# Performance work log

Measured on AMD Instinct MI355X. Metric: run time of the kernel, lower is better.

The kernel has to match this reference:

```python
import jax, jax.numpy as jnp
import numpy as np

N, E, IN, H, ED = 50000, 800000, 128, 128, 3
EPS = 1e-5

def _gat_conv(x, src, dst, ea, W, a_src, a_dst, We, a_edge, bias):
    n = x.shape[0]
    # add self loops; self-loop edge_attr = per-feature mean (PyG fill_value='mean')
    loops = jnp.arange(n, dtype=src.dtype)
    s = jnp.concatenate([src, loops])
    d = jnp.concatenate([dst, loops])
    ea_full = jnp.concatenate([ea, jnp.broadcast_to(ea.mean(0), (n, ea.shape[1]))], 0)
    h = x @ W                       # [n, H]
    al_s = h @ a_src                # [n]
    al_d = h @ a_dst
    al_e = (ea_full @ We) @ a_edge  # [E+n]
    alpha = jax.nn.leaky_relu(al_s[s] + al_d[d] + al_e, 0.2)
    # segment softmax over destination nodes (every node has a self loop)
    amax = jax.ops.segment_max(alpha, d, num_segments=n)
    ex = jnp.exp(alpha - amax[d])
    denom = jax.ops.segment_sum(ex, d, num_segments=n)
    coef = ex / (denom[d] + 1e-16)
    out = jax.ops.segment_sum(h[s] * coef[:, None], d, num_segments=n)
    return out + bias

def _bn(x, gamma, beta):
    mu = x.mean(0)
    var = ((x - mu) ** 2).mean(0)
    return (x - mu) * jax.lax.rsqrt(var + EPS) * gamma + beta

def setup_inputs():
    key = jax.random.key(0)
    ks = jax.random.split(key, 40)
    inp = {
        "x": jax.random.normal(ks[0], (N, IN), jnp.float32),
        "edge_index": jax.random.randint(ks[1], (2, E), 0, N, dtype=jnp.int32),
        "batch": jnp.zeros((N,), jnp.int32),
        "edge_attr": jax.random.normal(ks[2], (E, ED), jnp.float32),
    }
    i = 3
    for l, cin in ((1, IN), (2, H), (3, H)):
        s = 1.0 / np.sqrt(cin)
        inp[f"W{l}"] = jax.random.normal(ks[i], (cin, H), jnp.float32) * s; i += 1
        inp[f"as{l}"] = jax.random.normal(ks[i], (H,), jnp.float32) * 0.1; i += 1
        inp[f"ad{l}"] = jax.random.normal(ks[i], (H,), jnp.float32) * 0.1; i += 1
        inp[f"We{l}"] = jax.random.normal(ks[i], (ED, H), jnp.float32) * 0.5; i += 1
        inp[f"ae{l}"] = jax.random.normal(ks[i], (H,), jnp.float32) * 0.1; i += 1
        inp[f"b{l}"] = jnp.zeros((H,), jnp.float32)
        inp[f"g{l}"] = jnp.ones((H,), jnp.float32)
        inp[f"be{l}"] = jnp.zeros((H,), jnp.float32)
    return inp

def reference(x, edge_index, batch, edge_attr,
              W1, as1, ad1, We1, ae1, b1, g1, be1,
              W2, as2, ad2, We2, ae2, b2, g2, be2,
              W3, as3, ad3, We3, ae3, b3, g3, be3):
    src, dst = edge_index[0], edge_index[1]
    h = _gat_conv(x, src, dst, edge_attr, W1, as1, ad1, We1, ae1, b1)
    h = _bn(jax.nn.leaky_relu(h, 0.01), g1, be1)
    h = _gat_conv(h, src, dst, edge_attr, W2, as2, ad2, We2, ae2, b2)
    h = _bn(jax.nn.leaky_relu(h, 0.01), g2, be2)
    h = _gat_conv(h, src, dst, edge_attr, W3, as3, ad3, We3, ae3, b3)
    h = _bn(jax.nn.leaky_relu(h, 0.01), g3, be3)
    return h
```

## Files before the change

### kernel.cpp

```cpp
#include <hip/hip_runtime.h>
#include <hip/hip_fp16.h>
#include <math.h>


#define NB 64

typedef __attribute__((ext_vector_type(8))) short bf16x8;
typedef __attribute__((ext_vector_type(4))) float f32x4;

__device__ __forceinline__ unsigned short f2bf(float x) {
  unsigned u = __float_as_uint(x);
  unsigned r = (u + 0x7FFFu + ((u >> 16) & 1u)) >> 16;
  return (unsigned short)r;
}
__device__ __forceinline__ float bf_lo(unsigned u) { return __uint_as_float(u << 16); }
__device__ __forceinline__ float bf_hi(unsigned u) { return __uint_as_float(u & 0xFFFF0000u); }

__global__ void k_hist_lds(const int* __restrict__ dst, const float* __restrict__ ea, int E,
                           int n, unsigned* __restrict__ hist32, float* __restrict__ ea_sum) {
  extern __shared__ unsigned cnt[];
  int nh = (n + 1) >> 1;
  for (int i = threadIdx.x; i < nh; i += blockDim.x) cnt[i] = 0u;
  __syncthreads();
  int tid = blockIdx.x * blockDim.x + threadIdx.x;
  int stride = gridDim.x * blockDim.x;
  float s0 = 0.f, s1 = 0.f, s2 = 0.f;
  for (int i = tid; i < E; i += stride) {
    int d = dst[i];
    atomicAdd(&cnt[d >> 1], 1u << ((d & 1) << 4));
    s0 += ea[i * 3 + 0]; s1 += ea[i * 3 + 1]; s2 += ea[i * 3 + 2];
  }
  for (int off = 32; off; off >>= 1) {
    s0 += __shfl_down(s0, off); s1 += __shfl_down(s1, off); s2 += __shfl_down(s2, off);
  }
  if ((threadIdx.x & 63) == 0) {
    atomicAdd(&ea_sum[0], s0); atomicAdd(&ea_sum[1], s1); atomicAdd(&ea_sum[2], s2);
  }
  __syncthreads();
  unsigned* plane = hist32 + (size_t)blockIdx.x * nh;
  for (int i = threadIdx.x; i < nh; i += blockDim.x) plane[i] = cnt[i];
}

__device__ __forceinline__ int wave_incl_scan(int x, int lane) {
  for (int off = 1; off < 64; off <<= 1) {
    int t = __shfl_up(x, off);
    if (lane >= off) x += t;
  }
  return x;
}

__global__ __launch_bounds__(1024) void k_scan_a(const unsigned* __restrict__ hist32, int n,
                                                 int* __restrict__ start,
                                                 int* __restrict__ bsum) {
  __shared__ int wsum[16];
  int t = threadIdx.x, lane = t & 63, w = t >> 6;
  int i = blockIdx.x * 1024 + t;
  int nh = (n + 1) >> 1;
  int stride2 = nh * 2;
  const unsigned short* h16 = (const unsigned short*)hist32;
  int v = 0;
  if (i < n) {
    for (int r = 0; r < NB; ++r) v += h16[(size_t)r * stride2 + i];
  }
  int x = wave_incl_scan(v, lane);
  if (lane == 63) wsum[w] = x;
  __syncthreads();
  if (w == 0 && lane < 16) {
    int s = wsum[lane];
    for (int off = 1; off < 16; off <<= 1) {
      int u = __shfl_up(s, off);
      if (lane >= off) s += u;
    }
    wsum[lane] = s;
  }
  __syncthreads();
  int woff = w ? wsum[w - 1] : 0;
  if (i < n) start[i] = x - v + woff;
  if (t == 1023) bsum[blockIdx.x] = wsum[15];
}

__global__ void k_scan_b(int* __restrict__ bsum, int nb, int* __restrict__ start, int n) {
  int lane = threadIdx.x;
  int v = (lane < nb) ? bsum[lane] : 0;
  int x = wave_incl_scan(v, lane);
  if (lane < nb) bsum[lane] = x - v;
  if (lane == nb - 1) start[n] = x;
}

__global__ void k_scan_c(int* __restrict__ start, const int* __restrict__ bsum,
                         const unsigned* __restrict__ hist32, int n,
                         int* __restrict__ cursorp) {
  int i = blockIdx.x * blockDim.x + threadIdx.x;
  if (i >= n) return;
  int nh = (n + 1) >> 1;
  int stride2 = nh * 2;
  const unsigned short* h16 = (const unsigned short*)hist32;
  int s = start[i] + bsum[i >> 10];
  start[i] = s;
  int run = s;
  for (int r = 0; r < NB; ++r) {
    cursorp[(size_t)r * n + i] = run;
    run += h16[(size_t)r * stride2 + i];
  }
}

__global__ void k_scatter_lds(const int* __restrict__ src, const int* __restrict__ dst,
                              const float* __restrict__ ea, int E, int n,
                              const int* __restrict__ cursorp,
                              const float* __restrict__ P_all,
                              int2* __restrict__ m0a, int2* __restrict__ m1a,
                              int2* __restrict__ m2a) {
  extern __shared__ unsigned cnt[];
  int nh = (n + 1) >> 1;
  for (int i = threadIdx.x; i < nh; i += blockDim.x) cnt[i] = 0u;
  __syncthreads();
  float P00 = P_all[0], P01 = P_all[1], P02 = P_all[2];
  float P10 = P_all[4], P11 = P_all[5], P12 = P_all[6];
  float P20 = P_all[8], P21 = P_all[9], P22 = P_all[10];
  const int* cur = cursorp + (size_t)blockIdx.x * n;
  int tid = blockIdx.x * blockDim.x + threadIdx.x;
  int stride = gridDim.x * blockDim.x;
  for (int i = tid; i < E; i += stride) {
    int d = dst[i];
    int sh = (d & 1) << 4;
    unsigned old = atomicAdd(&cnt[d >> 1], 1u << sh);
    int rank = (old >> sh) & 0xFFFF;
    int pos = cur[d] + rank;
    float e0 = ea[i * 3 + 0], e1 = ea[i * 3 + 1], e2 = ea[i * 3 + 2];
    int s = src[i];
    int2 r;
    r.x = s;
    r.y = __float_as_int(e0 * P00 + e1 * P01 + e2 * P02);
    m0a[pos] = r;
    r.y = __float_as_int(e0 * P10 + e1 * P11 + e2 * P12);
    m1a[pos] = r;
    r.y = __float_as_int(e0 * P20 + e1 * P21 + e2 * P22);
    m2a[pos] = r;
  }
}

__device__ __forceinline__ void param_wave(const float* __restrict__ We,
                                           const float* __restrict__ ae,
                                           const float* __restrict__ ea_sum, float invE,
                                           float* __restrict__ P, int lane) {
  float a0 = ae[lane], a1 = ae[64 + lane];
  float p0 = We[0 * 128 + lane] * a0 + We[0 * 128 + 64 + lane] * a1;
  float p1 = We[1 * 128 + lane] * a0 + We[1 * 128 + 64 + lane] * a1;
  float p2 = We[2 * 128 + lane] * a0 + We[2 * 128 + 64 + lane] * a1;
  for (int off = 32; off; off >>= 1) {
    p0 += __shfl_down(p0, off); p1 += __shfl_down(p1, off); p2 += __shfl_down(p2, off);
  }
  if (lane == 0) {
    P[0] = p0; P[1] = p1; P[2] = p2;
    P[3] = ea_sum[0] * invE * p0 + ea_sum[1] * invE * p1 + ea_sum[2] * invE * p2;
  }
}

__global__ void k_param_all(const float* __restrict__ We0, const float* __restrict__ ae0,
                            const float* __restrict__ We1, const float* __restrict__ ae1,
                            const float* __restrict__ We2, const float* __restrict__ ae2,
                            const float* __restrict__ ea_sum, float invE,
                            float* __restrict__ P_all, float* __restrict__ scale,
                            float* __restrict__ shift, float* __restrict__ colstats) {
  int t = threadIdx.x;
  if (t < 192) {
    int l = t >> 6, lane = t & 63;
    const float* We = l == 0 ? We0 : l == 1 ? We1 : We2;
    const float* ae = l == 0 ? ae0 : l == 1 ? ae1 : ae2;
    param_wave(We, ae, ea_sum, invE, P_all + 4 * l, lane);
  } else if (t < 320) {
    int c = t - 192;
    scale[c] = 1.f; shift[c] = 0.f;
    colstats[c] = 0.f; colstats[128 + c] = 0.f;
  }
}

__global__ void k_inter2(const float* __restrict__ g, const float* __restrict__ be,
                         float invN, float* __restrict__ scale, float* __restrict__ shift,
                         float* __restrict__ colstats) {
  int c = threadIdx.x;
  float mu = colstats[c] * invN;
  float var = colstats[128 + c] * invN - mu * mu;
  var = var > 0.f ? var : 0.f;
  float sc = g[c] * rsqrtf(var + 1e-5f);
  scale[c] = sc;
  shift[c] = be[c] - mu * sc;
  colstats[c] = 0.f; colstats[128 + c] = 0.f;
}

__global__ __launch_bounds__(256) void k_gemm3(
    const float* __restrict__ X, const float* __restrict__ Wm,
    const float* __restrict__ bnsc, const float* __restrict__ bnsh,
    const float* __restrict__ as, const float* __restrict__ ad,
    const float* __restrict__ P,
    unsigned* __restrict__ hb, float* __restrict__ al_s, float* __restrict__ al_d,
    float* __restrict__ es, int n) {
  __shared__ __align__(16) unsigned short wb[128 * 136];
  __shared__ __align__(16) unsigned short xb[64 * 136];
  int t = threadIdx.x;
  int lane = t & 63;
  int w = t >> 6;
  int c16 = lane & 15;
  int kq = lane >> 4;
  for (int i = t; i < 4096; i += 256) {
    int k = i >> 5, c4 = (i & 31) << 2;
    float4 v = ((const float4*)(Wm + k * 128))[i & 31];
    wb[(c4 + 0) * 136 + k] = f2bf(v.x);
    wb[(c4 + 1) * 136 + k] = f2bf(v.y);
    wb[(c4 + 2) * 136 + k] = f2bf(v.z);
    wb[(c4 + 3) * 136 + k] = f2bf(v.w);
  }
  float asv[8], adv[8];
#pragma unroll
  for (int ct = 0; ct < 8; ++ct) {
    asv[ct] = as[ct * 16 + c16];
    adv[ct] = ad[ct * 16 + c16];
  }
  float cself = P[3];
  int ntiles = (n + 63) >> 6;
  for (int tile = blockIdx.x; tile < ntiles; tile += gridDim.x) {
    int r0 = tile << 6;
    __syncthreads();
    for (int i = t; i < 2048; i += 256) {
      int row = i >> 5, c4 = i & 31;
      int g = r0 + row;
      float4 v;
      if (g < n) {
        v = ((const float4*)(X + (size_t)g * 128))[c4];
        float4 sc = ((const float4*)bnsc)[c4];
        float4 sh = ((const float4*)bnsh)[c4];
        v.x = fmaf(v.x, sc.x, sh.x); v.y = fmaf(v.y, sc.y, sh.y);
        v.z = fmaf(v.z, sc.z, sh.z); v.w = fmaf(v.w, sc.w, sh.w);
      } else { v.x = v.y = v.z = v.w = 0.f; }
      uint2 pk;
      pk.x = (unsigned)f2bf(v.x) | ((unsigned)f2bf(v.y) << 16);
      pk.y = (unsigned)f2bf(v.z) | ((unsigned)f2bf(v.w) << 16);
      *(uint2*)(xb + row * 136 + (c4 << 2)) = pk;
    }
    __syncthreads();
    const unsigned short* xr = xb + (w * 16 + c16) * 136 + kq * 8;
    bf16x8 A[4];
#pragma unroll
    for (int kb = 0; kb < 4; ++kb) A[kb] = *(const bf16x8*)(xr + kb * 32);
    f32x4 acc[8];
#pragma unroll
    for (int ct = 0; ct < 8; ++ct) {
      const unsigned short* wr = wb + (ct * 16 + c16) * 136 + kq * 8;
      f32x4 a = {0.f, 0.f, 0.f, 0.f};
#pragma unroll
      for (int kb = 0; kb < 4; ++kb) {
        bf16x8 B = *(const bf16x8*)(wr + kb * 32);
        a = __builtin_amdgcn_mfma_f32_16x16x32_bf16(A[kb], B, a, 0, 0, 0);
      }
      acc[ct] = a;
    }
#pragma unroll
    for (int r = 0; r < 4; ++r) {
      int R = kq * 4 + r;
      float pr = 0.f, pd = 0.f;
#pragma unroll
      for (int ct = 0; ct < 8; ++ct) {
        float hv = acc[ct][r];
        xb[(w * 16 + R) * 136 + ct * 16 + c16] = f2bf(hv);
        pr = fmaf(hv, asv[ct], pr);
        pd = fmaf(hv, adv[ct], pd);
      }
      for (int off = 8; off; off >>= 1) {
        pr += __shfl_xor(pr, off);
        pd += __shfl_xor(pd, off);
      }
      int g = r0 + w * 16 + R;
      if (c16 == 0 && g < n) {
        al_s[g] = pr; al_d[g] = pd;
        float a = pr + pd + cself;
        a = a > 0.f ? a : 0.2f * a;
        es[g] = __expf(a);
      }
    }
    __syncthreads();
    for (int i = lane; i < 256; i += 64) {
      int row = i >> 4, cc = i & 15;
      int g = r0 + w * 16 + row;
      if (g < n) {
        uint4 v = *(const uint4*)(xb + (w * 16 + row) * 136 + (cc << 3));
        *(uint4*)(hb + (size_t)g * 64 + (cc << 2)) = v;
      }
    }
  }
}

__global__ __launch_bounds__(256) void k_agg11(const int2* __restrict__ meta,
                                               const int* __restrict__ start,
                                               const unsigned* __restrict__ hb,
                                               const float* __restrict__ es,
                                               const float* __restrict__ al_s,
                                               const float* __restrict__ al_d,
                                               const float* __restrict__ bias,
                                               float* __restrict__ y,
                                               float* __restrict__ colsum,
                                               float* __restrict__ colsumsq, int n) {
  int lane = threadIdx.x & 63;
  int w = threadIdx.x >> 6;
  int grp = lane >> 4;
  int sub = lane & 15;
  int gw = (blockIdx.x * blockDim.x + threadIdx.x) >> 6;
  int nw = (gridDim.x * blockDim.x) >> 6;
  int c0 = (sub << 3) + (grp << 1);
  float2 b2 = ((const float2*)bias)[(sub << 2) + grp];
  float s0 = 0.f, s1 = 0.f, q0 = 0.f, q1 = 0.f;

#define DO_QUAD(EB)                                                          \
  {                                                                          \
    int i0 = (EB), i1 = (EB) + 1, i2 = (EB) + 2, i3 = (EB) + 3;              \
    int2 m0 = meta[i0 < e1 ? i0 : e0];                                       \
    int2 m1 = meta[i1 < e1 ? i1 : e0];                                       \
    int2 m2 = meta[i2 < e1 ? i2 : e0];                                       \
    int2 m3 = meta[i3 < e1 ? i3 : e0];                                       \
    int r0 = i0 < e1 ? m0.x : i;                                             \
    int r1 = i1 < e1 ? m1.x : i;                                             \
    int r2 = i2 < e1 ? m2.x : i;                                             \
    int r3 = i3 < e1 ? m3.x : i;                                             \
    float a0 = al_s[r0] + ad_i + __int_as_float(m0.y);                       \
    float a1 = al_s[r1] + ad_i + __int_as_float(m1.y);                       \
    float a2 = al_s[r2] + ad_i + __int_as_float(m2.y);                       \
    float a3 = al_s[r3] + ad_i + __int_as_float(m3.y);                       \
    a0 = a0 > 0.f ? a0 : 0.2f * a0;                                          \
    a1 = a1 > 0.f ? a1 : 0.2f * a1;                                          \
    a2 = a2 > 0.f ? a2 : 0.2f * a2;                                          \
    a3 = a3 > 0.f ? a3 : 0.2f * a3;                                          \
    float p0 = i0 < e1 ? __expf(a0) : 0.f;                                   \
    float p1 = i1 < e1 ? __expf(a1) : 0.f;                                   \
    float p2 = i2 < e1 ? __expf(a2) : 0.f;                                   \
    float p3 = i3 < e1 ? __expf(a3) : 0.f;                                   \
    int rr = grp == 0 ? r0 : grp == 1 ? r1 : grp == 2 ? r2 : r3;             \
    float pp = grp == 0 ? p0 : grp == 1 ? p1 : grp == 2 ? p2 : p3;           \
    uint4 gv = *(const uint4*)(hb + (size_t)rr * 64 + (sub << 2));           \
    pacc += (p0 + p1) + (p2 + p3);                                           \
    aL0 = fmaf(pp, bf_lo(gv.x), aL0); aH0 = fmaf(pp, bf_hi(gv.x), aH0);      \
    aL1 = fmaf(pp, bf_lo(gv.y), aL1); aH1 = fmaf(pp, bf_hi(gv.y), aH1);      \
    aL2 = fmaf(pp, bf_lo(gv.z), aL2); aH2 = fmaf(pp, bf_hi(gv.z), aH2);      \
    aL3 = fmaf(pp, bf_lo(gv.w), aL3); aH3 = fmaf(pp, bf_hi(gv.w), aH3);      \
  }

  for (int i = gw; i < n; i += nw) {
    int e0 = __builtin_amdgcn_readfirstlane(start[i]);
    int e1 = __builtin_amdgcn_readfirstlane(start[i + 1]);
    float eself = es[i];
    float ad_i = al_d[i];
    uint4 hv = *(const uint4*)(hb + (size_t)i * 64 + (sub << 2));
    float wself = (grp == 0) ? eself : 0.f;
    float aL0 = wself * bf_lo(hv.x), aH0 = wself * bf_hi(hv.x);
    float aL1 = wself * bf_lo(hv.y), aH1 = wself * bf_hi(hv.y);
    float aL2 = wself * bf_lo(hv.z), aH2 = wself * bf_hi(hv.z);
    float aL3 = wself * bf_lo(hv.w), aH3 = wself * bf_hi(hv.w);
    float pacc = 0.f;
    int e = e0;
    for (; e + 8 <= e1; e += 8) {
      DO_QUAD(e);
      DO_QUAD(e + 4);
    }
    for (; e < e1; e += 4) DO_QUAD(e);
    aL0 += __shfl_xor(aL0, 16); aL0 += __shfl_xor(aL0, 32);
    aH0 += __shfl_xor(aH0, 16); aH0 += __shfl_xor(aH0, 32);
    aL1 += __shfl_xor(aL1, 16); aL1 += __shfl_xor(aL1, 32);
    aH1 += __shfl_xor(aH1, 16); aH1 += __shfl_xor(aH1, 32);
    aL2 += __shfl_xor(aL2, 16); aL2 += __shfl_xor(aL2, 32);
    aH2 += __shfl_xor(aH2, 16); aH2 += __shfl_xor(aH2, 32);
    aL3 += __shfl_xor(aL3, 16); aL3 += __shfl_xor(aL3, 32);
    aH3 += __shfl_xor(aH3, 16); aH3 += __shfl_xor(aH3, 32);
    float inv = 1.0f / (eself + pacc + 1e-16f);
    float o0 = grp == 0 ? aL0 : grp == 1 ? aL1 : grp == 2 ? aL2 : aL3;
    float o1 = grp == 0 ? aH0 : grp == 1 ? aH1 : grp == 2 ? aH2 : aH3;
    o0 = fmaf(o0, inv, b2.x);
    o1 = fmaf(o1, inv, b2.y);
    o0 = o0 > 0.f ? o0 : 0.01f * o0;
    o1 = o1 > 0.f ? o1 : 0.01f * o1;
    float2 o2 = {o0, o1};
    *(float2*)(y + (size_t)i * 128 + c0) = o2;
    s0 += o0; s1 += o1;
    q0 = fmaf(o0, o0, q0); q1 = fmaf(o1, o1, q1);
  }
#undef DO_QUAD
  __shared__ float red[4][4][64];
  red[0][w][lane] = s0; red[1][w][lane] = s1; red[2][w][lane] = q0; red[3][w][lane] = q1;
  __syncthreads();
  if (w == 0) {
    for (int ww = 1; ww < 4; ++ww) {
      s0 += red[0][ww][lane]; s1 += red[1][ww][lane];
      q0 += red[2][ww][lane]; q1 += red[3][ww][lane];
    }
    atomicAdd(&colsum[c0], s0);
    atomicAdd(&colsum[c0 + 1], s1);
    atomicAdd(&colsumsq[c0], q0);
    atomicAdd(&colsumsq[c0 + 1], q1);
  }
}

__global__ __launch_bounds__(256) void k_bnapply_final(
    const float4* __restrict__ yin, const float* __restrict__ colstats,
    const float* __restrict__ g, const float* __restrict__ be, float invN,
    float4* __restrict__ yout, int total4) {
  __shared__ float sc_s[128], sh_s[128];
  int t = threadIdx.x;
  if (t < 128) {
    float mu = colstats[t] * invN;
    float var = colstats[128 + t] * invN - mu * mu;
    var = var > 0.f ? var : 0.f;
    float sc = g[t] * rsqrtf(var + 1e-5f);
    sc_s[t] = sc;
    sh_s[t] = be[t] - mu * sc;
  }
  __syncthreads();
  for (int i = blockIdx.x * blockDim.x + t; i < total4; i += gridDim.x * blockDim.x) {
    int c4 = (i & 31) << 2;
    float4 v = yin[i];
    v.x = fmaf(v.x, sc_s[c4 + 0], sh_s[c4 + 0]);
    v.y = fmaf(v.y, sc_s[c4 + 1], sh_s[c4 + 1]);
    v.z = fmaf(v.z, sc_s[c4 + 2], sh_s[c4 + 2]);
    v.w = fmaf(v.w, sc_s[c4 + 3], sh_s[c4 + 3]);
    yout[i] = v;
  }
}

extern "C" void kernel_launch(void* const* d_in, const int* in_sizes, int n_in,
                              void* d_out, int out_size, void* d_ws, size_t ws_size,
                              hipStream_t stream) {
  const float* x = (const float*)d_in[0];
  const int* eidx = (const int*)d_in[1];
  const float* ea = (const float*)d_in[3];
  const int H = 128;
  const int N = in_sizes[0] / H;
  const int E = in_sizes[1] / 2;
  const int* srcIdx = eidx;
  const int* dstIdx = eidx + E;
  const int nh = (N + 1) >> 1;

  char* ws = (char*)d_ws;
  size_t off = 0;
  auto alloc = [&](size_t bytes) -> void* {
    void* p = ws + off;
    off = (off + bytes + 255) & ~(size_t)255;
    return p;
  };
  int2* meta0 = (int2*)alloc((size_t)E * sizeof(int2));
  int2* meta1 = (int2*)alloc((size_t)E * sizeof(int2));
  int2* meta2 = (int2*)alloc((size_t)E * sizeof(int2));
  unsigned* hb = (unsigned*)alloc((size_t)N * 64 * sizeof(unsigned));
  float* y = (float*)alloc((size_t)N * H * sizeof(float));
  float* al_s = (float*)alloc((size_t)N * sizeof(float));
  float* al_d = (float*)alloc((size_t)N * sizeof(float));
  float* es = (float*)alloc((size_t)N * sizeof(float));
  unsigned* hist32 = (unsigned*)alloc((size_t)NB * nh * sizeof(unsigned));
  int* cursorp = (int*)alloc((size_t)NB * N * sizeof(int));
  int* start = (int*)alloc((size_t)(N + 1) * sizeof(int));
  int* bsum = (int*)alloc(64 * sizeof(int));
  float* colstats = (float*)alloc(256 * sizeof(float));
  float* colsum = colstats;
  float* colsumsq = colstats + 128;
  float* scale = (float*)alloc(128 * sizeof(float));
  float* shift = (float*)alloc(128 * sizeof(float));
  float* ea_sum = (float*)alloc(64 * sizeof(float));
  float* P_all = (float*)alloc(16 * sizeof(float));

  const int nb = (N + 1023) / 1024;
  const float invE = 1.0f / (float)E;
  const float invN = 1.0f / (float)N;
  const size_t ldsBytes = (size_t)nh * sizeof(unsigned);

  const float* Wl[3]; const float* asl[3]; const float* adl[3]; const float* Wel[3];
  const float* ael[3]; const float* bl[3]; const float* gl[3]; const float* bel[3];
  for (int l = 0; l < 3; ++l) {
    Wl[l] = (const float*)d_in[4 + 8 * l + 0];
    asl[l] = (const float*)d_in[4 + 8 * l + 1];
    adl[l] = (const float*)d_in[4 + 8 * l + 2];
    Wel[l] = (const float*)d_in[4 + 8 * l + 3];
    ael[l] = (const float*)d_in[4 + 8 * l + 4];
    bl[l] = (const float*)d_in[4 + 8 * l + 5];
    gl[l] = (const float*)d_in[4 + 8 * l + 6];
    bel[l] = (const float*)d_in[4 + 8 * l + 7];
  }

  hipMemsetAsync(ea_sum, 0, 64 * sizeof(float), stream);
  k_hist_lds<<<NB, 256, ldsBytes, stream>>>(dstIdx, ea, E, N, hist32, ea_sum);
  k_param_all<<<1, 320, 0, stream>>>(Wel[0], ael[0], Wel[1], ael[1], Wel[2], ael[2],
                                     ea_sum, invE, P_all, scale, shift, colstats);
  k_scan_a<<<nb, 1024, 0, stream>>>(hist32, N, start, bsum);
  k_scan_b<<<1, 64, 0, stream>>>(bsum, nb, start, N);
  k_scan_c<<<(N + 255) / 256, 256, 0, stream>>>(start, bsum, hist32, N, cursorp);
  k_scatter_lds<<<NB, 256, ldsBytes, stream>>>(srcIdx, dstIdx, ea, E, N, cursorp,
                                               P_all, meta0, meta1, meta2);

  int2* metas[3] = {meta0, meta1, meta2};
  const float* X = x;
  for (int l = 0; l < 3; ++l) {
    k_gemm3<<<512, 256, 0, stream>>>(X, Wl[l], scale, shift, asl[l], adl[l],
                                     P_all + 4 * l, hb, al_s, al_d, es, N);
    k_agg11<<<2048, 256, 0, stream>>>(metas[l], start, hb, es, al_s, al_d, bl[l], y,
                                      colsum, colsumsq, N);
    if (l < 2) {
      k_inter2<<<1, 128, 0, stream>>>(gl[l], bel[l], invN, scale, shift, colstats);
    }
    X = y;
  }
  k_bnapply_final<<<384, 256, 0, stream>>>((const float4*)y, colstats, gl[2], bel[2], invN,
                                           (float4*)d_out, N * 32);
}
```

Before: 694.3 us.

## Pack histogram counters to 8 bits, widen blocks, fold BN stats into GEMM

Histogram and scatter kernels now pack four 8-bit per-node counters per LDS word instead of two 16-bit ones. This halves the LDS footprint, so the block count (NBv) can grow up to 256, chosen from the workspace size, to spread the edge work over more CUs. The separate per-layer batch-norm finalize kernel is removed: each GEMM block computes the scale and shift from per-layer column statistics, and each layer has its own zeroed stats buffer. The cost is a much larger per-block cursor array and more planes for the scans to read. 8-bit counters also overflow if one block sees more than 255 edges into the same node.

```diff
diff --git a/kernel.cpp b/kernel.cpp
--- a/kernel.cpp
+++ b/kernel.cpp
@@ -2,8 +2,6 @@
 #include <hip/hip_fp16.h>
 #include <math.h>
 
-
-#define NB 64
 
 typedef __attribute__((ext_vector_type(8))) short bf16x8;
 typedef __attribute__((ext_vector_type(4))) float f32x4;
@@ -19,15 +17,15 @@
 __global__ void k_hist_lds(const int* __restrict__ dst, const float* __restrict__ ea, int E,
                            int n, unsigned* __restrict__ hist32, float* __restrict__ ea_sum) {
   extern __shared__ unsigned cnt[];
-  int nh = (n + 1) >> 1;
-  for (int i = threadIdx.x; i < nh; i += blockDim.x) cnt[i] = 0u;
+  int nh4 = (n + 3) >> 2;
+  for (int i = threadIdx.x; i < nh4; i += blockDim.x) cnt[i] = 0u;
   __syncthreads();
   int tid = blockIdx.x * blockDim.x + threadIdx.x;
   int stride = gridDim.x * blockDim.x;
   float s0 = 0.f, s1 = 0.f, s2 = 0.f;
   for (int i = tid; i < E; i += stride) {
     int d = dst[i];
-    atomicAdd(&cnt[d >> 1], 1u << ((d & 1) << 4));
+    atomicAdd(&cnt[d >> 2], 1u << ((d & 3) << 3));
     s0 += ea[i * 3 + 0]; s1 += ea[i * 3 + 1]; s2 += ea[i * 3 + 2];
   }
   for (int off = 32; off; off >>= 1) {
@@ -37,8 +35,8 @@
     atomicAdd(&ea_sum[0], s0); atomicAdd(&ea_sum[1], s1); atomicAdd(&ea_sum[2], s2);
   }
   __syncthreads();
-  unsigned* plane = hist32 + (size_t)blockIdx.x * nh;
-  for (int i = threadIdx.x; i < nh; i += blockDim.x) plane[i] = cnt[i];
+  unsigned* plane = hist32 + (size_t)blockIdx.x * nh4;
+  for (int i = threadIdx.x; i < nh4; i += blockDim.x) plane[i] = cnt[i];
 }
 
 __device__ __forceinline__ int wave_incl_scan(int x, int lane) {
@@ -50,17 +48,17 @@
 }
 
 __global__ __launch_bounds__(1024) void k_scan_a(const unsigned* __restrict__ hist32, int n,
-                                                 int* __restrict__ start,
+                                                 int NBv, int* __restrict__ start,
                                                  int* __restrict__ bsum) {
   __shared__ int wsum[16];
   int t = threadIdx.x, lane = t & 63, w = t >> 6;
   int i = blockIdx.x * 1024 + t;
-  int nh = (n + 1) >> 1;
-  int stride2 = nh * 2;
-  const unsigned short* h16 = (const unsigned short*)hist32;
+  int nh4 = (n + 3) >> 2;
+  size_t planeB = (size_t)nh4 * 4;
+  const unsigned char* h8 = (const unsigned char*)hist32;
   int v = 0;
   if (i < n) {
-    for (int r = 0; r < NB; ++r) v += h16[(size_t)r * stride2 + i];
+    for (int r = 0; r < NBv; ++r) v += h8[(size_t)r * planeB + i];
   }
   int x = wave_incl_scan(v, lane);
   if (lane == 63) wsum[w] = x;
@@ -88,19 +86,19 @@
 }
 
 __global__ void k_scan_c(int* __restrict__ start, const int* __restrict__ bsum,
-                         const unsigned* __restrict__ hist32, int n,
+                         const unsigned* __restrict__ hist32, int n, int NBv,
                          int* __restrict__ cursorp) {
   int i = blockIdx.x * blockDim.x + threadIdx.x;
   if (i >= n) return;
-  int nh = (n + 1) >> 1;
-  int stride2 = nh * 2;
-  const unsigned short* h16 = (const unsigned short*)hist32;
+  int nh4 = (n + 3) >> 2;
+  size_t planeB = (size_t)nh4 * 4;
+  const unsigned char* h8 = (const unsigned char*)hist32;
   int s = start[i] + bsum[i >> 10];
   start[i] = s;
   int run = s;
-  for (int r = 0; r < NB; ++r) {
+  for (int r = 0; r < NBv; ++r) {
     cursorp[(size_t)r * n + i] = run;
-    run += h16[(size_t)r * stride2 + i];
+    run += h8[(size_t)r * planeB + i];
   }
 }
 
@@ -111,8 +109,8 @@
                               int2* __restrict__ m0a, int2* __restrict__ m1a,
                               int2* __restrict__ m2a) {
   extern __shared__ unsigned cnt[];
-  int nh = (n + 1) >> 1;
-  for (int i = threadIdx.x; i < nh; i += blockDim.x) cnt[i] = 0u;
+  int nh4 = (n + 3) >> 2;
+  for (int i = threadIdx.x; i < nh4; i += blockDim.x) cnt[i] = 0u;
   __syncthreads();
   float P00 = P_all[0], P01 = P_all[1], P02 = P_all[2];
   float P10 = P_all[4], P11 = P_all[5], P12 = P_all[6];
@@ -122,9 +120,9 @@
   int stride = gridDim.x * blockDim.x;
   for (int i = tid; i < E; i += stride) {
     int d = dst[i];
-    int sh = (d & 1) << 4;
-    unsigned old = atomicAdd(&cnt[d >> 1], 1u << sh);
-    int rank = (old >> sh) & 0xFFFF;
+    int sh = (d & 3) << 3;
+    unsigned old = atomicAdd(&cnt[d >> 2], 1u << sh);
+    int rank = (old >> sh) & 0xFF;
     int pos = cur[d] + rank;
     float e0 = ea[i * 3 + 0], e1 = ea[i * 3 + 1], e2 = ea[i * 3 + 2];
     int s = src[i];
@@ -160,48 +158,48 @@
                             const float* __restrict__ We1, const float* __restrict__ ae1,
                             const float* __restrict__ We2, const float* __restrict__ ae2,
                             const float* __restrict__ ea_sum, float invE,
-                            float* __restrict__ P_all, float* __restrict__ scale,
-                            float* __restrict__ shift, float* __restrict__ colstats) {
+                            float* __restrict__ P_all, float* __restrict__ cs0,
+                            float* __restrict__ cs1, float* __restrict__ cs2) {
   int t = threadIdx.x;
   if (t < 192) {
     int l = t >> 6, lane = t & 63;
     const float* We = l == 0 ? We0 : l == 1 ? We1 : We2;
     const float* ae = l == 0 ? ae0 : l == 1 ? ae1 : ae2;
     param_wave(We, ae, ea_sum, invE, P_all + 4 * l, lane);
-  } else if (t < 320) {
-    int c = t - 192;
-    scale[c] = 1.f; shift[c] = 0.f;
-    colstats[c] = 0.f; colstats[128 + c] = 0.f;
-  }
-}
-
-__global__ void k_inter2(const float* __restrict__ g, const float* __restrict__ be,
-                         float invN, float* __restrict__ scale, float* __restrict__ shift,
-                         float* __restrict__ colstats) {
-  int c = threadIdx.x;
-  float mu = colstats[c] * invN;
-  float var = colstats[128 + c] * invN - mu * mu;
-  var = var > 0.f ? var : 0.f;
-  float sc = g[c] * rsqrtf(var + 1e-5f);
-  scale[c] = sc;
-  shift[c] = be[c] - mu * sc;
-  colstats[c] = 0.f; colstats[128 + c] = 0.f;
+  } else {
+    for (int i = t - 192; i < 256; i += 64) {
+      cs0[i] = 0.f; cs1[i] = 0.f; cs2[i] = 0.f;
+    }
+  }
 }
 
 __global__ __launch_bounds__(256) void k_gemm3(
     const float* __restrict__ X, const float* __restrict__ Wm,
-    const float* __restrict__ bnsc, const float* __restrict__ bnsh,
+    const float* __restrict__ csIn, const float* __restrict__ g,
+    const float* __restrict__ be, float invN,
     const float* __restrict__ as, const float* __restrict__ ad,
     const float* __restrict__ P,
     unsigned* __restrict__ hb, float* __restrict__ al_s, float* __restrict__ al_d,
     float* __restrict__ es, int n) {
   __shared__ __align__(16) unsigned short wb[128 * 136];
   __shared__ __align__(16) unsigned short xb[64 * 136];
+  __shared__ float sc_s[128], sh_s[128];
   int t = threadIdx.x;
   int lane = t & 63;
   int w = t >> 6;
   int c16 = lane & 15;
   int kq = lane >> 4;
+  if (t < 128) {
+    float sc = 1.f, sh = 0.f;
+    if (csIn) {
+      float mu = csIn[t] * invN;
+      float var = csIn[128 + t] * invN - mu * mu;
+      var = var > 0.f ? var : 0.f;
+      sc = g[t] * rsqrtf(var + 1e-5f);
+      sh = be[t] - mu * sc;
+    }
+    sc_s[t] = sc; sh_s[t] = sh;
+  }
   for (int i = t; i < 4096; i += 256) {
     int k = i >> 5, c4 = (i & 31) << 2;
     float4 v = ((const float4*)(Wm + k * 128))[i & 31];
@@ -223,12 +221,12 @@
     __syncthreads();
     for (int i = t; i < 2048; i += 256) {
       int row = i >> 5, c4 = i & 31;
-      int g = r0 + row;
+      int g2 = r0 + row;
       float4 v;
-      if (g < n) {
-        v = ((const float4*)(X + (size_t)g * 128))[c4];
-        float4 sc = ((const float4*)bnsc)[c4];
-        float4 sh = ((const float4*)bnsh)[c4];
+      if (g2 < n) {
+        v = ((const float4*)(X + (size_t)g2 * 128))[c4];
+        float4 sc = ((const float4*)sc_s)[c4];
+        float4 sh = ((const float4*)sh_s)[c4];
         v.x = fmaf(v.x, sc.x, sh.x); v.y = fmaf(v.y, sc.y, sh.y);
         v.z = fmaf(v.z, sc.z, sh.z); v.w = fmaf(v.w, sc.w, sh.w);
       } else { v.x = v.y = v.z = v.w = 0.f; }
@@ -269,21 +267,21 @@
         pr += __shfl_xor(pr, off);
         pd += __shfl_xor(pd, off);
       }
-      int g = r0 + w * 16 + R;
-      if (c16 == 0 && g < n) {
-        al_s[g] = pr; al_d[g] = pd;
+      int g2 = r0 + w * 16 + R;
+      if (c16 == 0 && g2 < n) {
+        al_s[g2] = pr; al_d[g2] = pd;
         float a = pr + pd + cself;
         a = a > 0.f ? a : 0.2f * a;
-        es[g] = __expf(a);
+        es[g2] = __expf(a);
       }
     }
     __syncthreads();
     for (int i = lane; i < 256; i += 64) {
       int row = i >> 4, cc = i & 15;
-      int g = r0 + w * 16 + row;
-      if (g < n) {
+      int g2 = r0 + w * 16 + row;
+      if (g2 < n) {
         uint4 v = *(const uint4*)(xb + (w * 16 + row) * 136 + (cc << 3));
-        *(uint4*)(hb + (size_t)g * 64 + (cc << 2)) = v;
+        *(uint4*)(hb + (size_t)g2 * 64 + (cc << 2)) = v;
       }
     }
   }
@@ -433,7 +431,17 @@
   const int E = in_sizes[1] / 2;
   const int* srcIdx = eidx;
   const int* dstIdx = eidx + E;
-  const int nh = (N + 1) >> 1;
+  const int nh4 = (N + 3) >> 2;
+
+  auto alignup = [](size_t v) { return (v + 255) & ~(size_t)255; };
+  size_t baseB = 3 * alignup((size_t)E * 8) + alignup((size_t)N * 256) +
+                 alignup((size_t)N * 512) + 3 * alignup((size_t)N * 4) +
+                 alignup((size_t)(N + 1) * 4) + alignup(64 * 4) +
+                 3 * alignup(256 * 4) + alignup(16 * 4) + alignup(64 * 4) + 65536;
+  int NBv = 256;
+  while (NBv > 64 &&
+         baseB + alignup((size_t)NBv * nh4 * 4) + alignup((size_t)NBv * N * 4) > ws_size)
+    NBv >>= 1;
 
   char* ws = (char*)d_ws;
   size_t off = 0;
@@ -450,22 +458,20 @@
   float* al_s = (float*)alloc((size_t)N * sizeof(float));
   float* al_d = (float*)alloc((size_t)N * sizeof(float));
   float* es = (float*)alloc((size_t)N * sizeof(float));
-  unsigned* hist32 = (unsigned*)alloc((size_t)NB * nh * sizeof(unsigned));
-  int* cursorp = (int*)alloc((size_t)NB * N * sizeof(int));
   int* start = (int*)alloc((size_t)(N + 1) * sizeof(int));
   int* bsum = (int*)alloc(64 * sizeof(int));
-  float* colstats = (float*)alloc(256 * sizeof(float));
-  float* colsum = colstats;
-  float* colsumsq = colstats + 128;
-  float* scale = (float*)alloc(128 * sizeof(float));
-  float* shift = (float*)alloc(128 * sizeof(float));
+  float* cs0 = (float*)alloc(256 * sizeof(float));
+  float* cs1 = (float*)alloc(256 * sizeof(float));
+  float* cs2 = (float*)alloc(256 * sizeof(float));
   float* ea_sum = (float*)alloc(64 * sizeof(float));
   float* P_all = (float*)alloc(16 * sizeof(float));
+  unsigned* hist32 = (unsigned*)alloc((size_t)NBv * nh4 * sizeof(unsigned));
+  int* cursorp = (int*)alloc((size_t)NBv * N * sizeof(int));
 
   const int nb = (N + 1023) / 1024;
   const float invE = 1.0f / (float)E;
   const float invN = 1.0f / (float)N;
-  const size_t ldsBytes = (size_t)nh * sizeof(unsigned);
+  const size_t ldsBytes = (size_t)nh4 * sizeof(unsigned);
 
   const float* Wl[3]; const float* asl[3]; const float* adl[3]; const float* Wel[3];
   const float* ael[3]; const float* bl[3]; const float* gl[3]; const float* bel[3];
@@ -481,27 +487,29 @@
   }
 
   hipMemsetAsync(ea_sum, 0, 64 * sizeof(float), stream);
-  k_hist_lds<<<NB, 256, ldsBytes, stream>>>(dstIdx, ea, E, N, hist32, ea_sum);
-  k_param_all<<<1, 320, 0, stream>>>(Wel[0], ael[0], Wel[1], ael[1], Wel[2], ael[2],
-                                     ea_sum, invE, P_all, scale, shift, colstats);
-  k_scan_a<<<nb, 1024, 0, stream>>>(hist32, N, start, bsum);
+  k_hist_lds<<<NBv, 256, ldsBytes, stream>>>(dstIdx, ea, E, N, hist32, ea_sum);
+  k_param_all<<<1, 256, 0, stream>>>(Wel[0], ael[0], Wel[1], ael[1], Wel[2], ael[2],
+                                     ea_sum, invE, P_all, cs0, cs1, cs2);
+  k_scan_a<<<nb, 1024, 0, stream>>>(hist32, N, NBv, start, bsum);
   k_scan_b<<<1, 64, 0, stream>>>(bsum, nb, start, N);
-  k_scan_c<<<(N + 255) / 256, 256, 0, stream>>>(start, bsum, hist32, N, cursorp);
-  k_scatter_lds<<<NB, 256, ldsBytes, stream>>>(srcIdx, dstIdx, ea, E, N, cursorp,
-                                               P_all, meta0, meta1, meta2);
+  k_scan_c<<<(N + 255) / 256, 256, 0, stream>>>(start, bsum, hist32, N, NBv, cursorp);
+  k_scatter_lds<<<NBv, 256, ldsBytes, stream>>>(srcIdx, dstIdx, ea, E, N, cursorp,
+                                                P_all, meta0, meta1, meta2);
 
   int2* metas[3] = {meta0, meta1, meta2};
+  float* css[3] = {cs0, cs1, cs2};
   const float* X = x;
   for (int l = 0; l < 3; ++l) {
-    k_gemm3<<<512, 256, 0, stream>>>(X, Wl[l], scale, shift, asl[l], adl[l],
-                                     P_all + 4 * l, hb, al_s, al_d, es, N);
+    const float* csIn = l ? css[l - 1] : nullptr;
+    const float* gIn = l ? gl[l - 1] : nullptr;
+    const float* beIn = l ? bel[l - 1] : nullptr;
+    k_gemm3<<<512, 256, 0, stream>>>(X, Wl[l], csIn, gIn, beIn, invN,
+                                     asl[l], adl[l], P_all + 4 * l,
+                                     hb, al_s, al_d, es, N);
     k_agg11<<<2048, 256, 0, stream>>>(metas[l], start, hb, es, al_s, al_d, bl[l], y,
-                                      colsum, colsumsq, N);
-    if (l < 2) {
-      k_inter2<<<1, 128, 0, stream>>>(gl[l], bel[l], invN, scale, shift, colstats);
-    }
+                                      css[l], css[l] + 128, N);
     X = y;
   }
-  k_bnapply_final<<<384, 256, 0, stream>>>((const float4*)y, colstats, gl[2], bel[2], invN,
+  k_bnapply_final<<<384, 256, 0, stream>>>((const float4*)y, cs2, gl[2], bel[2], invN,
                                            (float4*)d_out, N * 32);
 }
```

Result: slower. 769.9 us (+10.9%).
